# Kernel optimization log

Hardware: AMD Instinct MI355X
Metric: run time of the kernel (lower is better)

## Reference

```python
import jax, jax.numpy as jnp
import numpy as np

N_NODES = 100000
N_EDGES = 1600000
F_IN = 128
HID = 128
N_CLS = 40


def setup_inputs() -> dict:
    key = jax.random.key(0)
    ks = jax.random.split(key, 8)
    x = jax.random.normal(ks[0], (N_NODES, F_IN), dtype=jnp.float32)
    edge_index = jax.random.randint(ks[1], (2, N_EDGES), 0, N_NODES, dtype=jnp.int32)
    s1 = 1.0 / np.sqrt(F_IN)
    s2 = 1.0 / np.sqrt(HID)
    W1 = jax.random.normal(ks[2], (F_IN, HID), dtype=jnp.float32) * s1
    b1 = jnp.zeros((HID,), dtype=jnp.float32)
    W2 = jax.random.normal(ks[3], (HID, HID), dtype=jnp.float32) * s2
    b2 = jnp.zeros((HID,), dtype=jnp.float32)
    Wout = jax.random.normal(ks[4], (HID, N_CLS), dtype=jnp.float32) * s2
    bout = jnp.zeros((N_CLS,), dtype=jnp.float32)
    return {"x": x, "edge_index": edge_index, "W1": W1, "b1": b1,
            "W2": W2, "b2": b2, "Wout": Wout, "bout": bout}


def gcn_conv(x, W, b, src, dst, n_nodes):
    """PyG-style GCNConv: h = D^-1/2 (A + I) D^-1/2 (x W) + b."""
    h = x @ W  # [N, H]
    # degree including self-loop
    deg = jnp.zeros((n_nodes,), dtype=h.dtype).at[dst].add(1.0) + 1.0
    dinv = jax.lax.rsqrt(deg)  # [N]
    coeff = dinv[src] * dinv[dst]  # [E]
    msgs = h[src] * coeff[:, None]  # [E, H] gathered messages
    agg = jnp.zeros_like(h).at[dst].add(msgs)
    # self-loop contribution: norm = dinv[i]^2
    agg = agg + h * (dinv * dinv)[:, None]
    return agg + b


def reference(x, edge_index, W1, b1, W2, b2, Wout, bout):
    src, dst = edge_index[0], edge_index[1]
    n = x.shape[0]
    h = jax.nn.relu(gcn_conv(x, W1, b1, src, dst, n))
    # dropout is identity in eval mode
    h = jax.nn.relu(gcn_conv(h, W2, b2, src, dst, n))
    return h @ Wout + bout
```

## Files before the change

kernel.cpp:

```cpp
#include <hip/hip_runtime.h>
#include <hip/hip_bf16.h>
#include <hip/hip_fp16.h>

#define NNODES 100000
#define NEDGES 1600000
#define FD 128
#define NCLS 40
#define DEGCAP 128
#define NBIN 256
#define BINW2 391
#define CAPB2 8192
#define SBLK 4096

typedef __attribute__((ext_vector_type(8))) short short8;
typedef __attribute__((ext_vector_type(4))) float floatx4;

__device__ __forceinline__ unsigned short f32_bf16_rn(float f) {
    unsigned u = __builtin_bit_cast(unsigned, f);
    u = u + 0x7fffu + ((u >> 16) & 1u);
    return (unsigned short)(u >> 16);
}
__device__ __forceinline__ float bf16_f32(unsigned short h) {
    unsigned u = ((unsigned)h) << 16;
    return __builtin_bit_cast(float, u);
}
__device__ __forceinline__ float4 h4_to_f4(int2 p) {
    __half2 a = __builtin_bit_cast(__half2, p.x);
    __half2 b = __builtin_bit_cast(__half2, p.y);
    float2 fa = __half22float2(a), fb = __half22float2(b);
    return make_float4(fa.x, fa.y, fb.x, fb.y);
}

__device__ __forceinline__ void pack_one(const float* __restrict__ W, int ncols,
                                         int nt_count, short* __restrict__ out,
                                         int id) {
    int lane = id & 63;
    int nt = (id >> 6) % nt_count;
    int ko = id / (64 * nt_count);
    int col = nt * 16 + (lane & 15);
    int kbase = ko * 32 + (lane >> 4) * 8;
    short* dst = out + (size_t)id * 16;
    #pragma unroll
    for (int j = 0; j < 8; ++j) {
        float v = (col < ncols) ? W[(size_t)(kbase + j) * ncols + col] : 0.f;
        unsigned short h = f32_bf16_rn(v);
        float r = v - bf16_f32(h);
        dst[j] = (short)h;
        dst[8 + j] = (short)f32_bf16_rn(r);
    }
}

__global__ __launch_bounds__(256) void prep(const float* __restrict__ W1,
                                            const float* __restrict__ W2,
                                            const float* __restrict__ Wout,
                                            short* __restrict__ w1pk,
                                            short* __restrict__ w2pk,
                                            short* __restrict__ wopk,
                                            int* __restrict__ cursor) {
    int id = blockIdx.x * blockDim.x + threadIdx.x;
    if (id < 2048) pack_one(W1, FD, 8, w1pk, id);
    else if (id < 4096) pack_one(W2, FD, 8, w2pk, id - 2048);
    else if (id < 4864) pack_one(Wout, NCLS, 3, wopk, id - 4096);
    else if (id < 4864 + NBIN) cursor[id - 4864] = (id - 4864) * CAPB2;
}

__global__ __launch_bounds__(256) void scatter_k(const int* __restrict__ src,
                                                 const int* __restrict__ dst,
                                                 int* __restrict__ cursor,
                                                 int* __restrict__ ebin) {
    __shared__ int lh[4][NBIN];
    __shared__ int obase[4][NBIN];
    int t = threadIdx.x, wv = t >> 6;
    int base = blockIdx.x * SBLK;
    for (int i = t; i < 4 * NBIN; i += 256) ((int*)lh)[i] = 0;
    __syncthreads();
    short bins[16]; short locs[16];
    #pragma unroll
    for (int i = 0; i < 16; ++i) {
        int idx = base + t + i * 256;
        int b = -1, loc = 0;
        if (idx < NEDGES) {
            int d = dst[idx];
            b = d / BINW2;
            loc = d - b * BINW2;
            atomicAdd(&lh[wv][b], 1);
        }
        bins[i] = (short)b; locs[i] = (short)loc;
    }
    __syncthreads();
    if (t < NBIN) {
        int c0 = lh[0][t], c1 = lh[1][t], c2 = lh[2][t], c3 = lh[3][t];
        int g = atomicAdd(&cursor[t], c0 + c1 + c2 + c3);
        obase[0][t] = g;
        obase[1][t] = g + c0;
        obase[2][t] = g + c0 + c1;
        obase[3][t] = g + c0 + c1 + c2;
    }
    __syncthreads();
    for (int i = t; i < 4 * NBIN; i += 256) ((int*)lh)[i] = 0;
    __syncthreads();
    #pragma unroll
    for (int i = 0; i < 16; ++i) {
        int idx = base + t + i * 256;
        if (idx < NEDGES) {
            int b = bins[i];
            int r = atomicAdd(&lh[wv][b], 1);
            int pos = obase[wv][b] + r;
            if (pos < (b + 1) * CAPB2)
                ebin[pos] = src[idx] | ((int)locs[i] << 17);
        }
    }
}

__global__ __launch_bounds__(256) void build_bin(const int* __restrict__ ebin,
                                                 const int* __restrict__ cursor,
                                                 int* __restrict__ adj,
                                                 int* __restrict__ rowptr,
                                                 int* __restrict__ degA,
                                                 float* __restrict__ dinv) {
    __shared__ int stage[CAPB2];
    __shared__ int hist[BINW2 + 1];
    __shared__ int rp[BINW2 + 1];
    int bin = blockIdx.x, t = threadIdx.x;
    int ne = cursor[bin] - bin * CAPB2;
    if (ne > CAPB2) ne = CAPB2;
    for (int i = t; i < ne; i += 256) stage[i] = ebin[bin * CAPB2 + i];
    for (int i = t; i < BINW2 + 1; i += 256) hist[i] = 0;
    __syncthreads();
    for (int i = t; i < ne; i += 256) atomicAdd(&hist[stage[i] >> 17], 1);
    __syncthreads();
    if (t < 64) {
        int c[7]; int s = 0;
        #pragma unroll
        for (int k = 0; k < 7; ++k) {
            int idx = t * 7 + k;
            c[k] = (idx < BINW2) ? hist[idx] : 0;
            s += c[k];
        }
        int inc = s;
        #pragma unroll
        for (int off = 1; off < 64; off <<= 1) {
            int o = __shfl_up(inc, off);
            if (t >= off) inc += o;
        }
        int excl = inc - s;
        #pragma unroll
        for (int k = 0; k < 7; ++k) {
            int idx = t * 7 + k;
            if (idx < BINW2) { rp[idx] = excl; excl += c[k]; }
        }
    }
    __syncthreads();
    int nbase = bin * BINW2;
    for (int l = t; l < BINW2; l += 256) {
        int node = nbase + l;
        if (node < NNODES) {
            rowptr[node] = bin * CAPB2 + rp[l];
            int dg = hist[l];
            degA[node] = dg;
            dinv[node] = rsqrtf((float)dg + 1.0f);
        }
    }
    __syncthreads();
    for (int i = t; i < BINW2 + 1; i += 256) hist[i] = 0;
    __syncthreads();
    for (int i = t; i < ne; i += 256) {
        int p = stage[i];
        int loc = p >> 17;
        int r = atomicAdd(&hist[loc], 1);
        adj[bin * CAPB2 + rp[loc] + r] = p & 0x1FFFF;
    }
}

__global__ __launch_bounds__(256) void gemm_mfma128_h(const float* __restrict__ X,
                                                      const short* __restrict__ Bpk,
                                                      __half* __restrict__ Y) {
    int w = threadIdx.x >> 6, lane = threadIdx.x & 63;
    int quad = lane >> 4, m = lane & 15;
    int row0 = blockIdx.x * 64 + w * 16;
    int arow = row0 + m;
    bool aok = arow < NNODES;
    floatx4 acc[8];
    #pragma unroll
    for (int nt = 0; nt < 8; ++nt) acc[nt] = (floatx4){0.f, 0.f, 0.f, 0.f};
    #pragma unroll
    for (int ko = 0; ko < 4; ++ko) {
        int kbase = ko * 32 + quad * 8;
        float4 a0 = aok ? *(const float4*)(X + (size_t)arow * FD + kbase)
                        : make_float4(0.f, 0.f, 0.f, 0.f);
        float4 a1 = aok ? *(const float4*)(X + (size_t)arow * FD + kbase + 4)
                        : make_float4(0.f, 0.f, 0.f, 0.f);
        float f[8] = {a0.x, a0.y, a0.z, a0.w, a1.x, a1.y, a1.z, a1.w};
        short8 ahi, alo;
        #pragma unroll
        for (int j = 0; j < 8; ++j) {
            unsigned short h = f32_bf16_rn(f[j]);
            ahi[j] = (short)h;
            alo[j] = (short)f32_bf16_rn(f[j] - bf16_f32(h));
        }
        const short* bp = Bpk + (size_t)(ko * 8) * 64 * 16 + (size_t)lane * 16;
        #pragma unroll
        for (int nt = 0; nt < 8; ++nt) {
            short8 bhi = *(const short8*)bp;
            short8 blo = *(const short8*)(bp + 8);
            bp += 64 * 16;
            acc[nt] = __builtin_amdgcn_mfma_f32_16x16x32_bf16(ahi, bhi, acc[nt], 0, 0, 0);
            acc[nt] = __builtin_amdgcn_mfma_f32_16x16x32_bf16(ahi, blo, acc[nt], 0, 0, 0);
            acc[nt] = __builtin_amdgcn_mfma_f32_16x16x32_bf16(alo, bhi, acc[nt], 0, 0, 0);
        }
    }
    #pragma unroll
    for (int r = 0; r < 4; ++r) {
        int rr = row0 + quad * 4 + r;
        if (rr < NNODES) {
            __half* y = Y + (size_t)rr * FD + m;
            #pragma unroll
            for (int nt = 0; nt < 8; ++nt) y[nt * 16] = __float2half(acc[nt][r]);
        }
    }
}

__global__ __launch_bounds__(256) void gemm_out_mfma(const float* __restrict__ X,
                                                     const short* __restrict__ Bpk,
                                                     const float* __restrict__ bout,
                                                     float* __restrict__ Y) {
    int w = threadIdx.x >> 6, lane = threadIdx.x & 63;
    int quad = lane >> 4, m = lane & 15;
    int row0 = blockIdx.x * 64 + w * 16;
    int arow = row0 + m;
    bool aok = arow < NNODES;
    floatx4 acc[3];
    #pragma unroll
    for (int nt = 0; nt < 3; ++nt) acc[nt] = (floatx4){0.f, 0.f, 0.f, 0.f};
    #pragma unroll
    for (int ko = 0; ko < 4; ++ko) {
        int kbase = ko * 32 + quad * 8;
        float4 a0 = aok ? *(const float4*)(X + (size_t)arow * FD + kbase)
                        : make_float4(0.f, 0.f, 0.f, 0.f);
        float4 a1 = aok ? *(const float4*)(X + (size_t)arow * FD + kbase + 4)
                        : make_float4(0.f, 0.f, 0.f, 0.f);
        float f[8] = {a0.x, a0.y, a0.z, a0.w, a1.x, a1.y, a1.z, a1.w};
        short8 ahi, alo;
        #pragma unroll
        for (int j = 0; j < 8; ++j) {
            unsigned short h = f32_bf16_rn(f[j]);
            ahi[j] = (short)h;
            alo[j] = (short)f32_bf16_rn(f[j] - bf16_f32(h));
        }
        const short* bp = Bpk + (size_t)(ko * 3) * 64 * 16 + (size_t)lane * 16;
        #pragma unroll
        for (int nt = 0; nt < 3; ++nt) {
            short8 bhi = *(const short8*)bp;
            short8 blo = *(const short8*)(bp + 8);
            bp += 64 * 16;
            acc[nt] = __builtin_amdgcn_mfma_f32_16x16x32_bf16(ahi, bhi, acc[nt], 0, 0, 0);
            acc[nt] = __builtin_amdgcn_mfma_f32_16x16x32_bf16(ahi, blo, acc[nt], 0, 0, 0);
            acc[nt] = __builtin_amdgcn_mfma_f32_16x16x32_bf16(alo, bhi, acc[nt], 0, 0, 0);
        }
    }
    #pragma unroll
    for (int r = 0; r < 4; ++r) {
        int rr = row0 + quad * 4 + r;
        if (rr < NNODES) {
            #pragma unroll
            for (int nt = 0; nt < 3; ++nt) {
                int col = nt * 16 + m;
                if (col < NCLS)
                    Y[(size_t)rr * NCLS + col] = acc[nt][r] + bout[col];
            }
        }
    }
}

__global__ __launch_bounds__(128) void aggregate_h(const int2* __restrict__ XW2,
                                                   const int* __restrict__ rowptr,
                                                   const int* __restrict__ degA,
                                                   const int* __restrict__ adj,
                                                   const float* __restrict__ dinv,
                                                   const float* __restrict__ bias,
                                                   float4* __restrict__ Y4) {
    __shared__ int ssrc[4][DEGCAP];
    __shared__ float scoef[4][DEGCAP];
    int sub  = threadIdx.x >> 5;
    int lane = threadIdx.x & 31;
    int node = blockIdx.x * 4 + sub;
    float di = dinv[node];
    int deg = degA[node];
    if (deg > DEGCAP) deg = DEGCAP;
    int base = rowptr[node];
    for (int j = lane; j < deg; j += 32) {
        int s = adj[base + j];
        ssrc[sub][j] = s;
        scoef[sub][j] = dinv[s] * di;
    }
    __syncthreads();
    float4 b = *(const float4*)(bias + 4 * lane);
    float4 v = h4_to_f4(XW2[(size_t)node * 32 + lane]);
    float sd = di * di;
    float4 acc;
    acc.x = v.x * sd; acc.y = v.y * sd; acc.z = v.z * sd; acc.w = v.w * sd;
    int j = 0;
    for (; j + 7 < deg; j += 8) {
        int2 p[8];
        float c[8];
        #pragma unroll
        for (int q = 0; q < 8; ++q) {
            p[q] = XW2[(size_t)ssrc[sub][j + q] * 32 + lane];
            c[q] = scoef[sub][j + q];
        }
        #pragma unroll
        for (int q = 0; q < 8; ++q) {
            float4 vq = h4_to_f4(p[q]);
            acc.x = fmaf(vq.x, c[q], acc.x); acc.y = fmaf(vq.y, c[q], acc.y);
            acc.z = fmaf(vq.z, c[q], acc.z); acc.w = fmaf(vq.w, c[q], acc.w);
        }
    }
    for (; j < deg; ++j) {
        float4 v0 = h4_to_f4(XW2[(size_t)ssrc[sub][j] * 32 + lane]);
        float c0 = scoef[sub][j];
        acc.x = fmaf(v0.x, c0, acc.x); acc.y = fmaf(v0.y, c0, acc.y);
        acc.z = fmaf(v0.z, c0, acc.z); acc.w = fmaf(v0.w, c0, acc.w);
    }
    acc.x = fmaxf(acc.x + b.x, 0.f);
    acc.y = fmaxf(acc.y + b.y, 0.f);
    acc.z = fmaxf(acc.z + b.z, 0.f);
    acc.w = fmaxf(acc.w + b.w, 0.f);
    Y4[(size_t)node * 32 + lane] = acc;
}

extern "C" void kernel_launch(void* const* d_in, const int* in_sizes, int n_in,
                              void* d_out, int out_size, void* d_ws, size_t ws_size,
                              hipStream_t stream) {
    const float* x    = (const float*)d_in[0];
    const int*   ei   = (const int*)d_in[1];
    const float* W1   = (const float*)d_in[2];
    const float* b1   = (const float*)d_in[3];
    const float* W2   = (const float*)d_in[4];
    const float* b2   = (const float*)d_in[5];
    const float* Wout = (const float*)d_in[6];
    const float* bout = (const float*)d_in[7];
    float* out = (float*)d_out;

    const int* srcv = ei;
    const int* dstv = ei + NEDGES;

    float* bufA   = (float*)d_ws;
    float* bufB   = bufA + (size_t)NNODES * FD;
    int*   adj    = (int*)(bufB + (size_t)NNODES * FD);
    int*   rowptr = adj + (size_t)NBIN * CAPB2;
    int*   degA   = rowptr + NNODES;
    float* dinv   = (float*)(degA + NNODES);
    short* w1pk   = (short*)(dinv + NNODES);
    short* w2pk   = w1pk + 2048 * 16;
    short* wopk   = w2pk + 2048 * 16;
    int*   cursor = (int*)(wopk + 768 * 16);
    int*   ebin   = (int*)bufA;
    __half* xwh   = (__half*)bufA;

    prep<<<20, 256, 0, stream>>>(W1, W2, Wout, w1pk, w2pk, wopk, cursor);

    scatter_k<<<(NEDGES + SBLK - 1) / SBLK, 256, 0, stream>>>(srcv, dstv, cursor, ebin);
    build_bin<<<NBIN, 256, 0, stream>>>(ebin, cursor, adj, rowptr, degA, dinv);

    const int gblocks = (NNODES + 63) / 64;
    gemm_mfma128_h<<<gblocks, 256, 0, stream>>>(x, w1pk, xwh);
    aggregate_h<<<NNODES / 4, 128, 0, stream>>>((const int2*)xwh, rowptr, degA,
                                                adj, dinv, b1, (float4*)bufB);
    gemm_mfma128_h<<<gblocks, 256, 0, stream>>>(bufB, w2pk, xwh);
    aggregate_h<<<NNODES / 4, 128, 0, stream>>>((const int2*)xwh, rowptr, degA,
                                                adj, dinv, b2, (float4*)bufB);
    gemm_out_mfma<<<gblocks, 256, 0, stream>>>(bufB, wopk, bout, out);
}
```

Measured before the change: 348.1 us.

## Store intermediate activations in fp16 and split edge-bin cursors per block group

The aggregation kernels now write post-ReLU activations as fp16 instead of fp32, and new GEMM variants read fp16 inputs. This halves the activation traffic between aggregation and the following GEMM. The scatter kernel now splits each destination bin into 8 sub-buckets keyed by block index. That spreads global atomic contention on the cursors and removes the second shared-memory histogram pass by reusing the ranks from the first pass. The risks are extra fp16 rounding of the activations and sub-bucket overflow, since each sub-bucket holds at most 1024 edges.

```diff
diff --git a/kernel.cpp b/kernel.cpp
--- a/kernel.cpp
+++ b/kernel.cpp
@@ -10,6 +10,7 @@
 #define NBIN 256
 #define BINW2 391
 #define CAPB2 8192
+#define SUBC 1024
 #define SBLK 4096
 
 typedef __attribute__((ext_vector_type(8))) short short8;
@@ -61,7 +62,10 @@
     if (id < 2048) pack_one(W1, FD, 8, w1pk, id);
     else if (id < 4096) pack_one(W2, FD, 8, w2pk, id - 2048);
     else if (id < 4864) pack_one(Wout, NCLS, 3, wopk, id - 4096);
-    else if (id < 4864 + NBIN) cursor[id - 4864] = (id - 4864) * CAPB2;
+    else if (id < 6912) {
+        int c = id - 4864;
+        cursor[c] = (c >> 3) * CAPB2 + (c & 7) * SUBC;
+    }
 }
 
 __global__ __launch_bounds__(256) void scatter_k(const int* __restrict__ src,
@@ -71,43 +75,42 @@
     __shared__ int lh[4][NBIN];
     __shared__ int obase[4][NBIN];
     int t = threadIdx.x, wv = t >> 6;
+    int g = blockIdx.x & 7;
     int base = blockIdx.x * SBLK;
     for (int i = t; i < 4 * NBIN; i += 256) ((int*)lh)[i] = 0;
     __syncthreads();
-    short bins[16]; short locs[16];
+    int pay[16];
+    unsigned short binv[16], rankv[16];
     #pragma unroll
     for (int i = 0; i < 16; ++i) {
         int idx = base + t + i * 256;
-        int b = -1, loc = 0;
+        int b = 0, r = 0, p = -1;
         if (idx < NEDGES) {
             int d = dst[idx];
             b = d / BINW2;
-            loc = d - b * BINW2;
-            atomicAdd(&lh[wv][b], 1);
-        }
-        bins[i] = (short)b; locs[i] = (short)loc;
+            p = src[idx] | ((d - b * BINW2) << 17);
+            r = atomicAdd(&lh[wv][b], 1);
+        }
+        pay[i] = p; binv[i] = (unsigned short)b; rankv[i] = (unsigned short)r;
     }
     __syncthreads();
     if (t < NBIN) {
         int c0 = lh[0][t], c1 = lh[1][t], c2 = lh[2][t], c3 = lh[3][t];
-        int g = atomicAdd(&cursor[t], c0 + c1 + c2 + c3);
-        obase[0][t] = g;
-        obase[1][t] = g + c0;
-        obase[2][t] = g + c0 + c1;
-        obase[3][t] = g + c0 + c1 + c2;
-    }
-    __syncthreads();
-    for (int i = t; i < 4 * NBIN; i += 256) ((int*)lh)[i] = 0;
+        int tot = c0 + c1 + c2 + c3;
+        int gb = tot ? atomicAdd(&cursor[t * 8 + g], tot) : 0;
+        obase[0][t] = gb;
+        obase[1][t] = gb + c0;
+        obase[2][t] = gb + c0 + c1;
+        obase[3][t] = gb + c0 + c1 + c2;
+    }
     __syncthreads();
     #pragma unroll
     for (int i = 0; i < 16; ++i) {
-        int idx = base + t + i * 256;
-        if (idx < NEDGES) {
-            int b = bins[i];
-            int r = atomicAdd(&lh[wv][b], 1);
-            int pos = obase[wv][b] + r;
-            if (pos < (b + 1) * CAPB2)
-                ebin[pos] = src[idx] | ((int)locs[i] << 17);
+        if (pay[i] != -1) {
+            int b = binv[i];
+            int pos = obase[wv][b] + rankv[i];
+            if (pos < b * CAPB2 + (g + 1) * SUBC)
+                ebin[pos] = pay[i];
         }
     }
 }
@@ -122,9 +125,16 @@
     __shared__ int hist[BINW2 + 1];
     __shared__ int rp[BINW2 + 1];
     int bin = blockIdx.x, t = threadIdx.x;
-    int ne = cursor[bin] - bin * CAPB2;
-    if (ne > CAPB2) ne = CAPB2;
-    for (int i = t; i < ne; i += 256) stage[i] = ebin[bin * CAPB2 + i];
+    int off = 0;
+    #pragma unroll
+    for (int x = 0; x < 8; ++x) {
+        int sb = bin * CAPB2 + x * SUBC;
+        int nex = cursor[bin * 8 + x] - sb;
+        if (nex > SUBC) nex = SUBC;
+        for (int i = t; i < nex; i += 256) stage[off + i] = ebin[sb + i];
+        off += nex;
+    }
+    int ne = off;
     for (int i = t; i < BINW2 + 1; i += 256) hist[i] = 0;
     __syncthreads();
     for (int i = t; i < ne; i += 256) atomicAdd(&hist[stage[i] >> 17], 1);
@@ -139,9 +149,9 @@
         }
         int inc = s;
         #pragma unroll
-        for (int off = 1; off < 64; off <<= 1) {
-            int o = __shfl_up(inc, off);
-            if (t >= off) inc += o;
+        for (int o = 1; o < 64; o <<= 1) {
+            int v = __shfl_up(inc, o);
+            if (t >= o) inc += v;
         }
         int excl = inc - s;
         #pragma unroll
@@ -220,10 +230,58 @@
     }
 }
 
-__global__ __launch_bounds__(256) void gemm_out_mfma(const float* __restrict__ X,
-                                                     const short* __restrict__ Bpk,
-                                                     const float* __restrict__ bout,
-                                                     float* __restrict__ Y) {
+__global__ __launch_bounds__(256) void gemm_mfma128_hh(const __half* __restrict__ X,
+                                                       const short* __restrict__ Bpk,
+                                                       __half* __restrict__ Y) {
+    int w = threadIdx.x >> 6, lane = threadIdx.x & 63;
+    int quad = lane >> 4, m = lane & 15;
+    int row0 = blockIdx.x * 64 + w * 16;
+    int arow = row0 + m;
+    bool aok = arow < NNODES;
+    floatx4 acc[8];
+    #pragma unroll
+    for (int nt = 0; nt < 8; ++nt) acc[nt] = (floatx4){0.f, 0.f, 0.f, 0.f};
+    #pragma unroll
+    for (int ko = 0; ko < 4; ++ko) {
+        int kbase = ko * 32 + quad * 8;
+        int4 ar = aok ? *(const int4*)(X + (size_t)arow * FD + kbase)
+                      : make_int4(0, 0, 0, 0);
+        float4 fa = h4_to_f4(make_int2(ar.x, ar.y));
+        float4 fb = h4_to_f4(make_int2(ar.z, ar.w));
+        float f[8] = {fa.x, fa.y, fa.z, fa.w, fb.x, fb.y, fb.z, fb.w};
+        short8 ahi, alo;
+        #pragma unroll
+        for (int j = 0; j < 8; ++j) {
+            unsigned short h = f32_bf16_rn(f[j]);
+            ahi[j] = (short)h;
+            alo[j] = (short)f32_bf16_rn(f[j] - bf16_f32(h));
+        }
+        const short* bp = Bpk + (size_t)(ko * 8) * 64 * 16 + (size_t)lane * 16;
+        #pragma unroll
+        for (int nt = 0; nt < 8; ++nt) {
+            short8 bhi = *(const short8*)bp;
+            short8 blo = *(const short8*)(bp + 8);
+            bp += 64 * 16;
+            acc[nt] = __builtin_amdgcn_mfma_f32_16x16x32_bf16(ahi, bhi, acc[nt], 0, 0, 0);
+            acc[nt] = __builtin_amdgcn_mfma_f32_16x16x32_bf16(ahi, blo, acc[nt], 0, 0, 0);
+            acc[nt] = __builtin_amdgcn_mfma_f32_16x16x32_bf16(alo, bhi, acc[nt], 0, 0, 0);
+        }
+    }
+    #pragma unroll
+    for (int r = 0; r < 4; ++r) {
+        int rr = row0 + quad * 4 + r;
+        if (rr < NNODES) {
+            __half* y = Y + (size_t)rr * FD + m;
+            #pragma unroll
+            for (int nt = 0; nt < 8; ++nt) y[nt * 16] = __float2half(acc[nt][r]);
+        }
+    }
+}
+
+__global__ __launch_bounds__(256) void gemm_out_mfma_h(const __half* __restrict__ X,
+                                                       const short* __restrict__ Bpk,
+                                                       const float* __restrict__ bout,
+                                                       float* __restrict__ Y) {
     int w = threadIdx.x >> 6, lane = threadIdx.x & 63;
     int quad = lane >> 4, m = lane & 15;
     int row0 = blockIdx.x * 64 + w * 16;
@@ -235,11 +293,11 @@
     #pragma unroll
     for (int ko = 0; ko < 4; ++ko) {
         int kbase = ko * 32 + quad * 8;
-        float4 a0 = aok ? *(const float4*)(X + (size_t)arow * FD + kbase)
-                        : make_float4(0.f, 0.f, 0.f, 0.f);
-        float4 a1 = aok ? *(const float4*)(X + (size_t)arow * FD + kbase + 4)
-                        : make_float4(0.f, 0.f, 0.f, 0.f);
-        float f[8] = {a0.x, a0.y, a0.z, a0.w, a1.x, a1.y, a1.z, a1.w};
+        int4 ar = aok ? *(const int4*)(X + (size_t)arow * FD + kbase)
+                      : make_int4(0, 0, 0, 0);
+        float4 fa = h4_to_f4(make_int2(ar.x, ar.y));
+        float4 fb = h4_to_f4(make_int2(ar.z, ar.w));
+        float f[8] = {fa.x, fa.y, fa.z, fa.w, fb.x, fb.y, fb.z, fb.w};
         short8 ahi, alo;
         #pragma unroll
         for (int j = 0; j < 8; ++j) {
@@ -278,7 +336,7 @@
                                                    const int* __restrict__ adj,
                                                    const float* __restrict__ dinv,
                                                    const float* __restrict__ bias,
-                                                   float4* __restrict__ Y4) {
+                                                   int2* __restrict__ Yh) {
     __shared__ int ssrc[4][DEGCAP];
     __shared__ float scoef[4][DEGCAP];
     int sub  = threadIdx.x >> 5;
@@ -321,11 +379,10 @@
         acc.x = fmaf(v0.x, c0, acc.x); acc.y = fmaf(v0.y, c0, acc.y);
         acc.z = fmaf(v0.z, c0, acc.z); acc.w = fmaf(v0.w, c0, acc.w);
     }
-    acc.x = fmaxf(acc.x + b.x, 0.f);
-    acc.y = fmaxf(acc.y + b.y, 0.f);
-    acc.z = fmaxf(acc.z + b.z, 0.f);
-    acc.w = fmaxf(acc.w + b.w, 0.f);
-    Y4[(size_t)node * 32 + lane] = acc;
+    __half2 h01 = __floats2half2_rn(fmaxf(acc.x + b.x, 0.f), fmaxf(acc.y + b.y, 0.f));
+    __half2 h23 = __floats2half2_rn(fmaxf(acc.z + b.z, 0.f), fmaxf(acc.w + b.w, 0.f));
+    Yh[(size_t)node * 32 + lane] = make_int2(__builtin_bit_cast(int, h01),
+                                             __builtin_bit_cast(int, h23));
 }
 
 extern "C" void kernel_launch(void* const* d_in, const int* in_sizes, int n_in,
@@ -356,8 +413,9 @@
     int*   cursor = (int*)(wopk + 768 * 16);
     int*   ebin   = (int*)bufA;
     __half* xwh   = (__half*)bufA;
-
-    prep<<<20, 256, 0, stream>>>(W1, W2, Wout, w1pk, w2pk, wopk, cursor);
+    __half* acth  = (__half*)bufB;
+
+    prep<<<27, 256, 0, stream>>>(W1, W2, Wout, w1pk, w2pk, wopk, cursor);
 
     scatter_k<<<(NEDGES + SBLK - 1) / SBLK, 256, 0, stream>>>(srcv, dstv, cursor, ebin);
     build_bin<<<NBIN, 256, 0, stream>>>(ebin, cursor, adj, rowptr, degA, dinv);
@@ -365,9 +423,9 @@
     const int gblocks = (NNODES + 63) / 64;
     gemm_mfma128_h<<<gblocks, 256, 0, stream>>>(x, w1pk, xwh);
     aggregate_h<<<NNODES / 4, 128, 0, stream>>>((const int2*)xwh, rowptr, degA,
-                                                adj, dinv, b1, (float4*)bufB);
-    gemm_mfma128_h<<<gblocks, 256, 0, stream>>>(bufB, w2pk, xwh);
+                                                adj, dinv, b1, (int2*)acth);
+    gemm_mfma128_hh<<<gblocks, 256, 0, stream>>>(acth, w2pk, xwh);
     aggregate_h<<<NNODES / 4, 128, 0, stream>>>((const int2*)xwh, rowptr, degA,
-                                                adj, dinv, b2, (float4*)bufB);
-    gemm_out_mfma<<<gblocks, 256, 0, stream>>>(bufB, wopk, bout, out);
-}
+                                                adj, dinv, b2, (int2*)acth);
+    gemm_out_mfma_h<<<gblocks, 256, 0, stream>>>(acth, wopk, bout, out);
+}
```

Result: faster. 337.7 us (-3.0%).
